# Kernel tuning notes

Hardware: AMD Instinct MI355X
Metric: run time of the kernel (lower is better)

The kernel has to match this reference:

```python
import jax, jax.numpy as jnp
import numpy as np

TAU = 2.0      # LIF membrane time constant
ALPHA = 4.0    # sigmoid surrogate sharpness (spikingjelly default)
EPS = 1e-5     # BatchNorm eps
HEADS = 8


def lif(x, vth):
    """MultiStepLIFNode: scan over leading time dim T. Hard reset to 0, detach_reset.
    Forward spike = heaviside(h - vth); backward uses sigmoid surrogate via straight-through."""
    def step(v, xt):
        h = v + (xt - v) / TAU
        hv = h - vth
        sg = jax.nn.sigmoid(ALPHA * hv)
        hard = (hv >= 0).astype(h.dtype)
        spike = sg + jax.lax.stop_gradient(hard - sg)
        v_new = h * (1.0 - jax.lax.stop_gradient(spike))  # detach_reset=True, v_reset=0
        return v_new, spike
    _, spikes = jax.lax.scan(step, jnp.zeros_like(x[0]), x)
    return spikes


def bn(x, gamma, beta, mean, var):
    # x: (T,B,C,N), params: (C,) ; eval-mode BatchNorm1d over channel axis 2
    inv = (gamma * jax.lax.rsqrt(var + EPS))[None, None, :, None]
    return (x - mean[None, None, :, None]) * inv + beta[None, None, :, None]


def setup_inputs() -> dict:
    key = jax.random.key(0)
    T, B, C, H, W = 4, 16, 384, 32, 32
    ks = jax.random.split(key, 24)
    d = {"x": jax.random.normal(ks[0], (T, B, C, H, W), jnp.float32)}
    i = 1
    wscale = 1.0 / np.sqrt(C)
    for p in ("q", "k", "v", "p"):
        d[p + "_w"] = jax.random.normal(ks[i], (C, C), jnp.float32) * wscale; i += 1
        d[p + "_gamma"] = jax.random.uniform(ks[i], (C,), jnp.float32, 0.5, 1.5); i += 1
        d[p + "_beta"] = jax.random.normal(ks[i], (C,), jnp.float32) * 0.1; i += 1
        d[p + "_mean"] = jax.random.normal(ks[i], (C,), jnp.float32) * 0.1; i += 1
        d[p + "_var"] = jax.random.uniform(ks[i], (C,), jnp.float32, 0.5, 1.5); i += 1
    d["p_bias"] = jax.random.normal(ks[i], (C,), jnp.float32) * 0.1
    return d


def reference(x, q_w, q_gamma, q_beta, q_mean, q_var,
              k_w, k_gamma, k_beta, k_mean, k_var,
              v_w, v_gamma, v_beta, v_mean, v_var,
              p_w, p_bias, p_gamma, p_beta, p_mean, p_var):
    T, B, C, H, W = x.shape
    N = H * W
    Ch = C // HEADS
    # input spiking (named proj_lif in source, applied first)
    xs = lif(x, 1.0).reshape(T, B, C, N)

    def branch(w, g, b, m, v):
        y = jnp.einsum('tbcn,dc->tbdn', xs, w)  # 1x1 Conv1d == channel matmul
        return lif(bn(y, g, b, m, v), 1.0).reshape(T, B, HEADS, Ch, N)

    q = branch(q_w, q_gamma, q_beta, q_mean, q_var)
    k = branch(k_w, k_gamma, k_beta, k_mean, k_var)
    v = branch(v_w, v_gamma, v_beta, v_mean, v_var)

    attn = jnp.sum(k * v, axis=3, keepdims=True)  # (T,B,h,1,N)
    attn = lif(attn, 0.5)
    out = (q * attn).reshape(T, B, C, N)
    out = jnp.einsum('tbcn,dc->tbdn', out, p_w) + p_bias[None, None, :, None]
    out = bn(out, p_gamma, p_beta, p_mean, p_var)
    return out.reshape(T, B, C, H, W)
```

## Files before the change

kernel.cpp:

```cpp
#include <hip/hip_runtime.h>

typedef unsigned short u16;
typedef unsigned char u8;
typedef unsigned int u32;
typedef float f32x4 __attribute__((ext_vector_type(4)));
typedef __bf16 bf16x8 __attribute__((ext_vector_type(8)));

#define SPB 6291456

__device__ __forceinline__ void gll16(const void* g, void* l) {
  __builtin_amdgcn_global_load_lds((const __attribute__((address_space(1))) void*)g,
                                   (__attribute__((address_space(3))) void*)l, 16, 0, 0);
}

__device__ __forceinline__ uint4 expand8f(uint2 v, u32 t) {
  u32 a = (v.x >> t) & 0x01010101u;
  u32 b = (v.y >> t) & 0x01010101u;
  uint4 r;
  r.x = __builtin_amdgcn_perm(0u, a, 0x0C010C00u) * 0x3F80u;
  r.y = __builtin_amdgcn_perm(0u, a, 0x0C030C02u) * 0x3F80u;
  r.z = __builtin_amdgcn_perm(0u, b, 0x0C010C00u) * 0x3F80u;
  r.w = __builtin_amdgcn_perm(0u, b, 0x0C030C02u) * 0x3F80u;
  return r;
}

__global__ __launch_bounds__(256) void k_convert(
    const float* __restrict__ qw, const float* __restrict__ kw,
    const float* __restrict__ vw, const float* __restrict__ pw,
    const float* __restrict__ qg, const float* __restrict__ qbt,
    const float* __restrict__ qm, const float* __restrict__ qv,
    const float* __restrict__ kg, const float* __restrict__ kbt,
    const float* __restrict__ km, const float* __restrict__ kv,
    const float* __restrict__ vg, const float* __restrict__ vbt,
    const float* __restrict__ vm, const float* __restrict__ vv,
    const float* __restrict__ pg, const float* __restrict__ pbt,
    const float* __restrict__ pm, const float* __restrict__ pv,
    const float* __restrict__ pbias,
    u16* __restrict__ Wstk, u16* __restrict__ Pw,
    float4* __restrict__ BNP, float4* __restrict__ PP) {
  int tid = blockIdx.x * 256 + threadIdx.x;
  if (tid < 442368) {
    int r = tid / 384, c = tid - r * 384;
    const float* src = (r < 384) ? qw : (r < 768) ? kw : vw;
    int rr = (r >= 768) ? r - 768 : (r >= 384) ? r - 384 : r;
    unsigned int u = __float_as_uint(src[rr * 384 + c]);
    u = (u + 0x7FFFu + ((u >> 16) & 1u)) >> 16;
    Wstk[tid] = (u16)u;
  } else if (tid < 589824) {
    int i = tid - 442368;
    unsigned int u = __float_as_uint(pw[i]);
    u = (u + 0x7FFFu + ((u >> 16) & 1u)) >> 16;
    Pw[i] = (u16)u;
  } else if (tid < 590976) {
    int r = tid - 589824;
    int br = r / 384, ch = r - br * 384;
    const float* g  = (br == 0) ? qg  : (br == 1) ? kg  : vg;
    const float* bt = (br == 0) ? qbt : (br == 1) ? kbt : vbt;
    const float* m  = (br == 0) ? qm  : (br == 1) ? km  : vm;
    const float* va = (br == 0) ? qv  : (br == 1) ? kv  : vv;
    float inv = g[ch] / sqrtf(va[ch] + 1e-5f);
    BNP[r] = make_float4(inv, m[ch], bt[ch], 0.f);
  } else if (tid < 591360) {
    int ch = tid - 590976;
    float inv = pg[ch] / sqrtf(pv[ch] + 1e-5f);
    PP[ch] = make_float4(inv, pm[ch], pbt[ch], pbias[ch]);
  }
}

__global__ __launch_bounds__(256) void k_lif_in(const float* __restrict__ x, u8* __restrict__ xsb) {
  const int nt = blockIdx.x, ct = blockIdx.y, b = blockIdx.z;
  const int tid = threadIdx.x;
  const int nj = tid & 63, cr = tid >> 6;
  const int c0 = ct * 64, n0 = nt * 64;
  __shared__ u32 nibs[64 * 65];
  float v[16];
  u32 nib[16];
  #pragma unroll
  for (int i = 0; i < 16; ++i) { v[i] = 0.f; nib[i] = 0u; }
  for (int t = 0; t < 4; ++t) {
    const float* xr = x + (((t * 16 + b) * 384 + c0 + cr) * 1024) + n0 + nj;
    #pragma unroll
    for (int it = 0; it < 16; ++it) {
      float xv = xr[it * 4096];
      float vv = v[it];
      float h = __fadd_rn(vv, __fmul_rn(__fsub_rn(xv, vv), 0.5f));
      bool s = h >= 1.f;
      v[it] = s ? 0.f : h;
      nib[it] |= (s ? 1u : 0u) << t;
    }
  }
  #pragma unroll
  for (int it = 0; it < 16; ++it) nibs[nj * 65 + cr + it * 4] = nib[it];
  __syncthreads();
  const int n = tid >> 2, ch = tid & 3;
  u32 w0[4];
  #pragma unroll
  for (int q = 0; q < 4; ++q) {
    u32 acc = 0;
    #pragma unroll
    for (int i = 0; i < 4; ++i)
      acc |= (nibs[n * 65 + ch * 16 + q * 4 + i] & 0xFu) << (8 * i);
    w0[q] = acc;
  }
  *(uint4*)(xsb + ((size_t)(b * 1024 + n0 + n)) * 384 + c0 + ch * 16) =
      make_uint4(w0[0], w0[1], w0[2], w0[3]);
}

#define XLDS_U16 13312
#define WSLOT_U16 4096

#define GISSUE(kt) gll16(Wp + (kt) * 32, &lds[XLDS_U16 + ((kt) % 6) * WSLOT_U16 + wst])

#define SYNCP(n) do { \
    asm volatile("s_waitcnt vmcnt(" #n ")" ::: "memory"); \
    __builtin_amdgcn_s_barrier(); \
    asm volatile("" ::: "memory"); \
  } while (0)

#define COMPUTE(kt) do { \
    const u8* xb_ = (const u8*)lds; \
    const u16* wb_ = &lds[XLDS_U16 + ((kt) % 6) * WSLOT_U16]; \
    bf16x8 ax[4]; \
    _Pragma("unroll") \
    for (int ji = 0; ji < 4; ++ji) { \
      uint2 xr_ = *(const uint2*)(xb_ + (wjg * 16 + ji * 4 + d4) * 416 + (kt) * 32 + g8); \
      uint4 e_ = expand8f(xr_, t_lane); \
      ax[ji] = *(bf16x8*)&e_; \
    } \
    __builtin_amdgcn_s_setprio(1); \
    _Pragma("unroll") \
    for (int ci = 0; ci < 4; ++ci) { \
      bf16x8 bw_ = *(const bf16x8*)&wb_[(wcg * 64 + ci * 16 + l15) * 32 + swoff]; \
      _Pragma("unroll") \
      for (int ji = 0; ji < 4; ++ji) \
        acc[ji][ci] = __builtin_amdgcn_mfma_f32_16x16x32_bf16(ax[ji], bw_, acc[ji][ci], 0, 0, 0); \
    } \
    __builtin_amdgcn_s_setprio(0); \
  } while (0)

#define GEMM_PIPELINE() do { \
    GISSUE(0); GISSUE(1); GISSUE(2); GISSUE(3); GISSUE(4); \
    SYNCP(4); GISSUE(5);  COMPUTE(0); \
    SYNCP(4); GISSUE(6);  COMPUTE(1); \
    SYNCP(4); GISSUE(7);  COMPUTE(2); \
    SYNCP(4); GISSUE(8);  COMPUTE(3); \
    SYNCP(4); GISSUE(9);  COMPUTE(4); \
    SYNCP(4); GISSUE(10); COMPUTE(5); \
    SYNCP(4); GISSUE(11); COMPUTE(6); \
    SYNCP(4); COMPUTE(7); \
    SYNCP(3); COMPUTE(8); \
    SYNCP(2); COMPUTE(9); \
    SYNCP(1); COMPUTE(10); \
    SYNCP(0); COMPUTE(11); \
  } while (0)

#define XSTAGE(XSRC) do { \
    const int xn_ = tid >> 3, xcp_ = tid & 7; \
    const u8* xs_ = (XSRC) + (size_t)(b * 1024 + jt * 64 + xn_) * 384 + xcp_ * 48; \
    u8* xd_ = (u8*)lds + xn_ * 416 + xcp_ * 48; \
    uint4 v0_ = *(const uint4*)(xs_); \
    uint4 v1_ = *(const uint4*)(xs_ + 16); \
    uint4 v2_ = *(const uint4*)(xs_ + 32); \
    *(uint4*)(xd_) = v0_; *(uint4*)(xd_ + 16) = v1_; *(uint4*)(xd_ + 32) = v2_; \
    __syncthreads(); \
  } while (0)

#define GEMM_SETUP() \
  const int tid = threadIdx.x; \
  const int w = tid >> 6, l = tid & 63; \
  const int wjg = w >> 1, wcg = w & 1; \
  const int l15 = tid & 15, g = l >> 4; \
  const int swoff = (g ^ ((l15 >> 1) & 3)) * 8; \
  const int wst = w * 512; \
  const int d4 = l15 >> 2, g8 = g * 8; \
  const u32 t_lane = (u32)(l15 & 3); \
  const int sch = (l & 3) ^ ((l >> 3) & 3); \
  f32x4 acc[4][4]; \
  { const f32x4 zero_ = {0.f, 0.f, 0.f, 0.f}; \
    _Pragma("unroll") \
    for (int ji = 0; ji < 4; ++ji) \
      _Pragma("unroll") \
      for (int ci = 0; ci < 4; ++ci) acc[ji][ci] = zero_; }

__global__ __launch_bounds__(512, 4) void k_qkv(
    const u16* __restrict__ Wstk, const u8* __restrict__ xsb,
    const float4* __restrict__ BNP, u8* __restrict__ sp) {
  const int jt = blockIdx.x, mt = blockIdx.y, b = blockIdx.z;
  __shared__ u16 lds[37888];

  GEMM_SETUP();
  XSTAGE(xsb);

  const int m0 = mt * 128;
  const u16* Wp = Wstk + (size_t)(m0 + w * 16 + (l >> 2)) * 384 + sch * 8;

  GEMM_PIPELINE();

  const int br = mt / 3;
  const int cb = (mt - br * 3) * 128;
  const int n_base = b * 1024 + jt * 64 + wjg * 16 + g;
  u8* spW = sp + (size_t)br * SPB;
  #pragma unroll
  for (int ci = 0; ci < 4; ++ci) {
    const int c_loc = wcg * 64 + ci * 16 + l15;
    float4 pr = BNP[br * 384 + cb + c_loc];
    #pragma unroll
    for (int ji = 0; ji < 4; ++ji) {
      f32x4 a = acc[ji][ci];
      u32 bits = 0;
      float vv = 0.f;
      #pragma unroll
      for (int t = 0; t < 4; ++t) {
        float z = __fadd_rn(__fmul_rn(__fsub_rn(a[t], pr.y), pr.x), pr.z);
        float h = __fadd_rn(vv, __fmul_rn(__fsub_rn(z, vv), 0.5f));
        bool s = h >= 1.f;
        vv = s ? 0.f : h;
        bits |= (s ? 1u : 0u) << t;
      }
      spW[(size_t)(n_base + ji * 4) * 384 + cb + c_loc] = (u8)bits;
    }
  }
}

__global__ __launch_bounds__(256) void k_attn(const u8* __restrict__ sp, u8* __restrict__ xpb) {
  const int gw = blockIdx.x * 4 + (threadIdx.x >> 6);
  const int l = threadIdx.x & 63;
  const int b = gw >> 10, n = gw & 1023;
  const u8* qB = sp;
  const u8* kB = sp + SPB;
  const u8* vB = sp + 2 * SPB;
  const int base = (b * 1024 + n) * 384 + l * 6;
  u16 qu[3], ku[3], vu[3];
  #pragma unroll
  for (int i = 0; i < 3; ++i) {
    qu[i] = *(const u16*)(qB + base + 2 * i);
    ku[i] = *(const u16*)(kB + base + 2 * i);
    vu[i] = *(const u16*)(vB + base + 2 * i);
  }
  u32 s = 0;
  #pragma unroll
  for (int i = 0; i < 3; ++i) {
    u32 a = (u32)(ku[i] & vu[i]);
    #pragma unroll
    for (int t = 0; t < 4; ++t) {
      u32 x = (a >> t) & 0x0101u;
      s += ((x + (x >> 8)) & 3u) << (8 * t);
    }
  }
  s += __shfl_xor(s, 1);
  s += __shfl_xor(s, 2);
  s += __shfl_xor(s, 4);
  float v = 0.f;
  u32 m8 = 0;
  #pragma unroll
  for (int t = 0; t < 4; ++t) {
    float attn = (float)((s >> (8 * t)) & 0xFFu);
    float h = __fadd_rn(v, __fmul_rn(__fsub_rn(attn, v), 0.5f));
    bool sk = h >= 0.5f;
    v = sk ? 0.f : h;
    m8 |= (sk ? 1u : 0u) << t;
  }
  const u16 mm = (u16)(m8 * 0x0101u);
  u16* dst = (u16*)(xpb + base);
  #pragma unroll
  for (int i = 0; i < 3; ++i) dst[i] = qu[i] & mm;
}

__global__ __launch_bounds__(512, 4) void k_proj(
    const u16* __restrict__ Pw, const u8* __restrict__ xpb,
    const float4* __restrict__ PP, float* __restrict__ out) {
  const int jt = blockIdx.x, mt = blockIdx.y, b = blockIdx.z;
  __shared__ u16 lds[37888];

  GEMM_SETUP();
  XSTAGE(xpb);

  const int m0 = mt * 128;
  const u16* Wp = Pw + (size_t)(m0 + w * 16 + (l >> 2)) * 384 + sch * 8;

  GEMM_PIPELINE();

  __syncthreads();
  float* scr = (float*)lds;
  const int n0im = jt * 64;
  float4 prc[4];
  #pragma unroll
  for (int ci = 0; ci < 4; ++ci) prc[ci] = PP[m0 + wcg * 64 + ci * 16 + l15];

  #pragma unroll
  for (int t = 0; t < 4; ++t) {
    #pragma unroll
    for (int ci = 0; ci < 4; ++ci) {
      const int c_loc = wcg * 64 + ci * 16 + l15;
      float4 pr = prc[ci];
      #pragma unroll
      for (int ji = 0; ji < 4; ++ji) {
        const int n_loc = wjg * 16 + ji * 4 + g;
        float zz = __fadd_rn(acc[ji][ci][t], pr.w);
        zz = __fadd_rn(__fmul_rn(__fsub_rn(zz, pr.y), pr.x), pr.z);
        scr[c_loc * 68 + n_loc] = zz;
      }
    }
    __syncthreads();
    #pragma unroll
    for (int it = 0; it < 4; ++it) {
      int slot = tid + it * 512;
      int c = slot >> 4, li = slot & 15;
      float4 val = *(const float4*)&scr[c * 68 + li * 4];
      *(float4*)&out[(((size_t)(t * 16 + b) * 384) + m0 + c) * 1024 + n0im + li * 4] = val;
    }
    __syncthreads();
  }
}

extern "C" void kernel_launch(void* const* d_in, const int* in_sizes, int n_in,
                              void* d_out, int out_size, void* d_ws, size_t ws_size,
                              hipStream_t stream) {
  (void)in_sizes; (void)n_in; (void)out_size; (void)ws_size;
  const float* x   = (const float*)d_in[0];
  const float* qw  = (const float*)d_in[1];
  const float* qg  = (const float*)d_in[2];
  const float* qbt = (const float*)d_in[3];
  const float* qm  = (const float*)d_in[4];
  const float* qv  = (const float*)d_in[5];
  const float* kw  = (const float*)d_in[6];
  const float* kg  = (const float*)d_in[7];
  const float* kbt = (const float*)d_in[8];
  const float* km  = (const float*)d_in[9];
  const float* kv  = (const float*)d_in[10];
  const float* vw  = (const float*)d_in[11];
  const float* vg  = (const float*)d_in[12];
  const float* vbt = (const float*)d_in[13];
  const float* vm  = (const float*)d_in[14];
  const float* vv  = (const float*)d_in[15];
  const float* pw  = (const float*)d_in[16];
  const float* pg  = (const float*)d_in[17];
  const float* pbt = (const float*)d_in[18];
  const float* pm  = (const float*)d_in[19];
  const float* pv  = (const float*)d_in[20];
  const float* pbias = (const float*)d_in[21];

  char* ws = (char*)d_ws;
  u8*  xsb   = (u8*)ws;
  u8*  sp    = (u8*)(ws + 6291456);
  u8*  xpb   = (u8*)(ws + 25165824);
  u16* Wstk  = (u16*)(ws + 31457280);
  u16* Pw    = (u16*)(ws + 32342016);
  float4* BNP = (float4*)(ws + 32636928);
  float4* PP  = (float4*)(ws + 32655360);

  k_convert<<<2310, 256, 0, stream>>>(qw, kw, vw, pw, qg, qbt, qm, qv, kg, kbt, km, kv,
                                      vg, vbt, vm, vv, pg, pbt, pm, pv, pbias,
                                      Wstk, Pw, BNP, PP);
  k_lif_in<<<dim3(16, 6, 16), 256, 0, stream>>>(x, xsb);
  k_qkv<<<dim3(16, 9, 16), 512, 0, stream>>>(Wstk, xsb, BNP, sp);
  k_attn<<<4096, 256, 0, stream>>>(sp, xpb);
  k_proj<<<dim3(16, 3, 16), 512, 0, stream>>>(Pw, xpb, PP, (float*)d_out);
}
```

Baseline: 123.1 us.

## Shrink weight ring to three slots and split MFMA phases with extra barriers

Reworks the GEMM pipeline so the weight staging buffer holds three K-slices instead of six. Each step now waits for only one outstanding load, issues the next, and splits the MFMA work into two halves separated by workgroup barriers. LDS per block shrinks, which may let more blocks share a CU, but prefetch depth drops and there are three barriers per K-step instead of one. This risks exposing global-load latency and adding sync stalls.

```diff
diff --git a/kernel.cpp b/kernel.cpp
--- a/kernel.cpp
+++ b/kernel.cpp
@@ -109,49 +109,58 @@
 #define XLDS_U16 13312
 #define WSLOT_U16 4096
 
-#define GISSUE(kt) gll16(Wp + (kt) * 32, &lds[XLDS_U16 + ((kt) % 6) * WSLOT_U16 + wst])
-
-#define SYNCP(n) do { \
-    asm volatile("s_waitcnt vmcnt(" #n ")" ::: "memory"); \
-    __builtin_amdgcn_s_barrier(); \
-    asm volatile("" ::: "memory"); \
-  } while (0)
-
-#define COMPUTE(kt) do { \
-    const u8* xb_ = (const u8*)lds; \
-    const u16* wb_ = &lds[XLDS_U16 + ((kt) % 6) * WSLOT_U16]; \
-    bf16x8 ax[4]; \
+#define GISSUE(kt) gll16(Wp + (kt) * 32, &lds[XLDS_U16 + ((kt) % 3) * WSLOT_U16 + wst])
+
+#define MFMA2CI(c0, c1) do { \
     _Pragma("unroll") \
-    for (int ji = 0; ji < 4; ++ji) { \
-      uint2 xr_ = *(const uint2*)(xb_ + (wjg * 16 + ji * 4 + d4) * 416 + (kt) * 32 + g8); \
-      uint4 e_ = expand8f(xr_, t_lane); \
-      ax[ji] = *(bf16x8*)&e_; \
-    } \
-    __builtin_amdgcn_s_setprio(1); \
-    _Pragma("unroll") \
-    for (int ci = 0; ci < 4; ++ci) { \
+    for (int ci = (c0); ci <= (c1); ++ci) { \
       bf16x8 bw_ = *(const bf16x8*)&wb_[(wcg * 64 + ci * 16 + l15) * 32 + swoff]; \
       _Pragma("unroll") \
       for (int ji = 0; ji < 4; ++ji) \
         acc[ji][ci] = __builtin_amdgcn_mfma_f32_16x16x32_bf16(ax[ji], bw_, acc[ji][ci], 0, 0, 0); \
     } \
+  } while (0)
+
+#define GSTEP(t, VN, ISS) do { \
+    asm volatile("s_waitcnt vmcnt(" #VN ")" ::: "memory"); \
+    __builtin_amdgcn_s_barrier(); \
+    asm volatile("" ::: "memory"); \
+    ISS; \
+    const u8* xb_ = (const u8*)lds; \
+    const u16* wb_ = &lds[XLDS_U16 + ((t) % 3) * WSLOT_U16]; \
+    bf16x8 ax[4]; \
+    _Pragma("unroll") \
+    for (int ji = 0; ji < 4; ++ji) { \
+      uint2 xr_ = *(const uint2*)(xb_ + (wjg * 16 + ji * 4 + d4) * 416 + (t) * 32 + g8); \
+      uint4 e_ = expand8f(xr_, t_lane); \
+      ax[ji] = *(bf16x8*)&e_; \
+    } \
+    __builtin_amdgcn_s_setprio(1); \
+    MFMA2CI(0, 1); \
     __builtin_amdgcn_s_setprio(0); \
+    __builtin_amdgcn_s_barrier(); \
+    asm volatile("" ::: "memory"); \
+    __builtin_amdgcn_s_setprio(1); \
+    MFMA2CI(2, 3); \
+    __builtin_amdgcn_s_setprio(0); \
+    __builtin_amdgcn_s_barrier(); \
+    asm volatile("" ::: "memory"); \
   } while (0)
 
 #define GEMM_PIPELINE() do { \
-    GISSUE(0); GISSUE(1); GISSUE(2); GISSUE(3); GISSUE(4); \
-    SYNCP(4); GISSUE(5);  COMPUTE(0); \
-    SYNCP(4); GISSUE(6);  COMPUTE(1); \
-    SYNCP(4); GISSUE(7);  COMPUTE(2); \
-    SYNCP(4); GISSUE(8);  COMPUTE(3); \
-    SYNCP(4); GISSUE(9);  COMPUTE(4); \
-    SYNCP(4); GISSUE(10); COMPUTE(5); \
-    SYNCP(4); GISSUE(11); COMPUTE(6); \
-    SYNCP(4); COMPUTE(7); \
-    SYNCP(3); COMPUTE(8); \
-    SYNCP(2); COMPUTE(9); \
-    SYNCP(1); COMPUTE(10); \
-    SYNCP(0); COMPUTE(11); \
+    GISSUE(0); GISSUE(1); \
+    GSTEP(0, 1, GISSUE(2)); \
+    GSTEP(1, 1, GISSUE(3)); \
+    GSTEP(2, 1, GISSUE(4)); \
+    GSTEP(3, 1, GISSUE(5)); \
+    GSTEP(4, 1, GISSUE(6)); \
+    GSTEP(5, 1, GISSUE(7)); \
+    GSTEP(6, 1, GISSUE(8)); \
+    GSTEP(7, 1, GISSUE(9)); \
+    GSTEP(8, 1, GISSUE(10)); \
+    GSTEP(9, 1, GISSUE(11)); \
+    GSTEP(10, 1, ); \
+    GSTEP(11, 0, ); \
   } while (0)
 
 #define XSTAGE(XSRC) do { \
@@ -186,7 +195,7 @@
     const u16* __restrict__ Wstk, const u8* __restrict__ xsb,
     const float4* __restrict__ BNP, u8* __restrict__ sp) {
   const int jt = blockIdx.x, mt = blockIdx.y, b = blockIdx.z;
-  __shared__ u16 lds[37888];
+  __shared__ u16 lds[25600];
 
   GEMM_SETUP();
   XSTAGE(xsb);
@@ -270,7 +279,7 @@
     const u16* __restrict__ Pw, const u8* __restrict__ xpb,
     const float4* __restrict__ PP, float* __restrict__ out) {
   const int jt = blockIdx.x, mt = blockIdx.y, b = blockIdx.z;
-  __shared__ u16 lds[37888];
+  __shared__ u16 lds[25600];
 
   GEMM_SETUP();
   XSTAGE(xpb);
```

New measurement: 128.9 us. +4.8%, slower.

## Fuse attention spike masking into projection GEMM staging and vectorize input LIF loads

Applied to the files above, without the earlier changes.

Removes the separate k_attn kernel: each k_proj block now computes the k·v per-head spike counts, the attention LIF, and the masked q tile directly from the QKV spike buffer, writing the result into LDS in place of XSTAGE. This saves a kernel launch and the write and re-read of the intermediate xpb buffer. In exchange, the attention work is repeated for each of the 3 output-channel tiles (mt), and the q/k/v loads sit in the prologue of the GEMM block. Separately, k_lif_in now reads x with float4 vector loads instead of scalar loads.

```diff
diff --git a/kernel.cpp b/kernel.cpp
--- a/kernel.cpp
+++ b/kernel.cpp
@@ -70,27 +70,36 @@
 __global__ __launch_bounds__(256) void k_lif_in(const float* __restrict__ x, u8* __restrict__ xsb) {
   const int nt = blockIdx.x, ct = blockIdx.y, b = blockIdx.z;
   const int tid = threadIdx.x;
-  const int nj = tid & 63, cr = tid >> 6;
+  const int n4 = tid & 15, cL = tid >> 4;
   const int c0 = ct * 64, n0 = nt * 64;
   __shared__ u32 nibs[64 * 65];
-  float v[16];
-  u32 nib[16];
-  #pragma unroll
-  for (int i = 0; i < 16; ++i) { v[i] = 0.f; nib[i] = 0u; }
+  float v[4][4];
+  u32 nib[4][4];
+  #pragma unroll
+  for (int it = 0; it < 4; ++it)
+    #pragma unroll
+    for (int ns = 0; ns < 4; ++ns) { v[it][ns] = 0.f; nib[it][ns] = 0u; }
   for (int t = 0; t < 4; ++t) {
-    const float* xr = x + (((t * 16 + b) * 384 + c0 + cr) * 1024) + n0 + nj;
-    #pragma unroll
-    for (int it = 0; it < 16; ++it) {
-      float xv = xr[it * 4096];
-      float vv = v[it];
-      float h = __fadd_rn(vv, __fmul_rn(__fsub_rn(xv, vv), 0.5f));
-      bool s = h >= 1.f;
-      v[it] = s ? 0.f : h;
-      nib[it] |= (s ? 1u : 0u) << t;
-    }
-  }
-  #pragma unroll
-  for (int it = 0; it < 16; ++it) nibs[nj * 65 + cr + it * 4] = nib[it];
+    #pragma unroll
+    for (int it = 0; it < 4; ++it) {
+      const float4 xv = *(const float4*)&x[(size_t)(((t * 16 + b) * 384 + c0 + cL + it * 16)) * 1024
+                                           + n0 + n4 * 4];
+      #pragma unroll
+      for (int ns = 0; ns < 4; ++ns) {
+        float xe = (ns == 0) ? xv.x : (ns == 1) ? xv.y : (ns == 2) ? xv.z : xv.w;
+        float vv = v[it][ns];
+        float h = __fadd_rn(vv, __fmul_rn(__fsub_rn(xe, vv), 0.5f));
+        bool s = h >= 1.f;
+        v[it][ns] = s ? 0.f : h;
+        nib[it][ns] |= (s ? 1u : 0u) << t;
+      }
+    }
+  }
+  #pragma unroll
+  for (int it = 0; it < 4; ++it)
+    #pragma unroll
+    for (int ns = 0; ns < 4; ++ns)
+      nibs[(n4 * 4 + ns) * 65 + cL + it * 16] = nib[it][ns];
   __syncthreads();
   const int n = tid >> 2, ch = tid & 3;
   u32 w0[4];
@@ -222,58 +231,63 @@
   }
 }
 
-__global__ __launch_bounds__(256) void k_attn(const u8* __restrict__ sp, u8* __restrict__ xpb) {
-  const int gw = blockIdx.x * 4 + (threadIdx.x >> 6);
-  const int l = threadIdx.x & 63;
-  const int b = gw >> 10, n = gw & 1023;
-  const u8* qB = sp;
-  const u8* kB = sp + SPB;
-  const u8* vB = sp + 2 * SPB;
-  const int base = (b * 1024 + n) * 384 + l * 6;
-  u16 qu[3], ku[3], vu[3];
-  #pragma unroll
-  for (int i = 0; i < 3; ++i) {
-    qu[i] = *(const u16*)(qB + base + 2 * i);
-    ku[i] = *(const u16*)(kB + base + 2 * i);
-    vu[i] = *(const u16*)(vB + base + 2 * i);
-  }
-  u32 s = 0;
-  #pragma unroll
-  for (int i = 0; i < 3; ++i) {
-    u32 a = (u32)(ku[i] & vu[i]);
-    #pragma unroll
-    for (int t = 0; t < 4; ++t) {
-      u32 x = (a >> t) & 0x0101u;
-      s += ((x + (x >> 8)) & 3u) << (8 * t);
-    }
-  }
-  s += __shfl_xor(s, 1);
-  s += __shfl_xor(s, 2);
-  s += __shfl_xor(s, 4);
-  float v = 0.f;
-  u32 m8 = 0;
-  #pragma unroll
-  for (int t = 0; t < 4; ++t) {
-    float attn = (float)((s >> (8 * t)) & 0xFFu);
-    float h = __fadd_rn(v, __fmul_rn(__fsub_rn(attn, v), 0.5f));
-    bool sk = h >= 0.5f;
-    v = sk ? 0.f : h;
-    m8 |= (sk ? 1u : 0u) << t;
-  }
-  const u16 mm = (u16)(m8 * 0x0101u);
-  u16* dst = (u16*)(xpb + base);
-  #pragma unroll
-  for (int i = 0; i < 3; ++i) dst[i] = qu[i] & mm;
-}
-
 __global__ __launch_bounds__(512, 4) void k_proj(
-    const u16* __restrict__ Pw, const u8* __restrict__ xpb,
+    const u16* __restrict__ Pw, const u8* __restrict__ sp,
     const float4* __restrict__ PP, float* __restrict__ out) {
   const int jt = blockIdx.x, mt = blockIdx.y, b = blockIdx.z;
   __shared__ u16 lds[37888];
 
+  {
+    const int tt = threadIdx.x;
+    const int xn_ = tt >> 3, hd_ = tt & 7;
+    const u8* qrow = sp + (size_t)(b * 1024 + jt * 64 + xn_) * 384 + hd_ * 48;
+    const u8* krow = qrow + SPB;
+    const u8* vrow = qrow + 2 * SPB;
+    u32 qa[12], ka[12], va[12];
+    #pragma unroll
+    for (int i = 0; i < 3; ++i) {
+      *(uint4*)&qa[i * 4] = *(const uint4*)(qrow + i * 16);
+      *(uint4*)&ka[i * 4] = *(const uint4*)(krow + i * 16);
+      *(uint4*)&va[i * 4] = *(const uint4*)(vrow + i * 16);
+    }
+    u32 m0 = 0, m1 = 0, m2 = 0, m3 = 0;
+    #pragma unroll
+    for (int i = 0; i < 12; ++i) {
+      u32 a = ka[i] & va[i];
+      m0 += a & 0x01010101u;
+      m1 += (a >> 1) & 0x01010101u;
+      m2 += (a >> 2) & 0x01010101u;
+      m3 += (a >> 3) & 0x01010101u;
+    }
+    float s0 = (float)((m0 * 0x01010101u) >> 24);
+    float s1 = (float)((m1 * 0x01010101u) >> 24);
+    float s2 = (float)((m2 * 0x01010101u) >> 24);
+    float s3 = (float)((m3 * 0x01010101u) >> 24);
+    float vv = 0.f;
+    u32 m8 = 0;
+    #pragma unroll
+    for (int t = 0; t < 4; ++t) {
+      float attn = (t == 0) ? s0 : (t == 1) ? s1 : (t == 2) ? s2 : s3;
+      float h = __fadd_rn(vv, __fmul_rn(__fsub_rn(attn, vv), 0.5f));
+      bool sk = h >= 0.5f;
+      vv = sk ? 0.f : h;
+      m8 |= (sk ? 1u : 0u) << t;
+    }
+    const u32 mm = m8 * 0x01010101u;
+    u8* xd_ = (u8*)lds + xn_ * 416 + hd_ * 48;
+    #pragma unroll
+    for (int i = 0; i < 3; ++i) {
+      uint4 wv;
+      wv.x = qa[i * 4 + 0] & mm;
+      wv.y = qa[i * 4 + 1] & mm;
+      wv.z = qa[i * 4 + 2] & mm;
+      wv.w = qa[i * 4 + 3] & mm;
+      *(uint4*)(xd_ + i * 16) = wv;
+    }
+    __syncthreads();
+  }
+
   GEMM_SETUP();
-  XSTAGE(xpb);
 
   const int m0 = mt * 128;
   const u16* Wp = Pw + (size_t)(m0 + w * 16 + (l >> 2)) * 384 + sch * 8;
@@ -343,7 +357,6 @@
   char* ws = (char*)d_ws;
   u8*  xsb   = (u8*)ws;
   u8*  sp    = (u8*)(ws + 6291456);
-  u8*  xpb   = (u8*)(ws + 25165824);
   u16* Wstk  = (u16*)(ws + 31457280);
   u16* Pw    = (u16*)(ws + 32342016);
   float4* BNP = (float4*)(ws + 32636928);
@@ -354,6 +367,5 @@
                                       Wstk, Pw, BNP, PP);
   k_lif_in<<<dim3(16, 6, 16), 256, 0, stream>>>(x, xsb);
   k_qkv<<<dim3(16, 9, 16), 512, 0, stream>>>(Wstk, xsb, BNP, sp);
-  k_attn<<<4096, 256, 0, stream>>>(sp, xpb);
-  k_proj<<<dim3(16, 3, 16), 512, 0, stream>>>(Pw, xpb, PP, (float*)d_out);
-}
+  k_proj<<<dim3(16, 3, 16), 512, 0, stream>>>(Pw, sp, PP, (float*)d_out);
+}
```

Result: faster. 119.0 us (-3.3%).
